# Kernel optimization log

Hardware: AMD Instinct MI355X
Metric: run time of the kernel (lower is better)

Reference implementation:

```python
import jax, jax.numpy as jnp
import numpy as np

N_NODES = 50000
N_EDGES = 800000
D = 128
N_LAYERS = 5  # 1 input + 3 hidden + 1 output MaxAggConv layers


def setup_inputs() -> dict:
    key = jax.random.key(0)
    k1, k2, k3, k4 = jax.random.split(key, 4)
    x = jax.random.normal(k1, (N_NODES, D), dtype=jnp.float32)
    edge_index = jax.random.randint(k2, (2, N_EDGES), 0, N_NODES, dtype=jnp.int64)
    # Linear params per layer (all layers are D->D here): W [out,in], b [out]
    Ws = jax.random.normal(k3, (N_LAYERS, D, D), dtype=jnp.float32) * (1.0 / np.sqrt(D))
    bs = jax.random.normal(k4, (N_LAYERS, D), dtype=jnp.float32) * 0.01
    return {"x": x, "edge_index": edge_index, "Ws": Ws, "bs": bs}


def _max_agg_conv(x, src, dst, W, b, n_nodes):
    # Linear: x @ W^T + b  (nn.Linear convention)
    h = jnp.einsum('nd,od->no', x, W) + b
    # gather per-edge messages x_j (source nodes), scatter-max into targets
    m = jax.ops.segment_max(h[src], dst, num_segments=n_nodes)
    # PyG scatter-max fills nodes with no incoming edges with 0
    return jnp.where(jnp.isneginf(m), 0.0, m)


def reference(x, edge_index, Ws, bs):
    src = edge_index[0]
    dst = edge_index[1]
    n = x.shape[0]
    for i in range(N_LAYERS - 1):
        x = _max_agg_conv(x, src, dst, Ws[i], bs[i], n)
        x = jax.nn.silu(x)
    x = _max_agg_conv(x, src, dst, Ws[N_LAYERS - 1], bs[N_LAYERS - 1], n)
    return x
```

## Files before the change

kernel.cpp:

```cpp
#include <hip/hip_runtime.h>
#include <hip/hip_bf16.h>
#include <hip/hip_fp16.h>
#include <math.h>

#define DF 128
#define NLAYERS 5

typedef __attribute__((ext_vector_type(8))) short bf16x8;
typedef __attribute__((ext_vector_type(4))) short short4v;
typedef __attribute__((ext_vector_type(4))) float f32x4;

__device__ inline unsigned short f2bf(float f) {
    unsigned u = __float_as_uint(f);
    u += 0x7FFF + ((u >> 16) & 1u);
    return (unsigned short)(u >> 16);
}
__device__ inline float bf2f(unsigned short s) {
    return __uint_as_float(((unsigned)s) << 16);
}

__device__ inline unsigned pkmax(unsigned a, unsigned b) {
    unsigned d;
    asm("v_pk_max_f16 %0, %1, %2" : "=v"(d) : "v"(a), "v"(b));
    return d;
}
__device__ inline float h2f(unsigned short u) {
    __half_raw r; r.x = u;
    return __half2float(__half(r));
}


__global__ void hist_rank_kernel(const int* __restrict__ dst, int* __restrict__ cnt,
        int* __restrict__ rank, int E) {
    int i = blockIdx.x * blockDim.x + threadIdx.x;
    if (i < E) rank[i] = atomicAdd(&cnt[dst[i]], 1);
}

__global__ __launch_bounds__(256) void partial_sum_kernel(const int* __restrict__ cnt,
        int* __restrict__ bsum, int n) {
    __shared__ int red[256];
    int t = threadIdx.x;
    int i = blockIdx.x * 256 + t;
    red[t] = (i < n) ? cnt[i] : 0;
    __syncthreads();
    for (int d = 128; d > 0; d >>= 1) {
        if (t < d) red[t] += red[t + d];
        __syncthreads();
    }
    if (t == 0) bsum[blockIdx.x] = red[0];
}

__global__ __launch_bounds__(1024) void scan_bsums_kernel(const int* __restrict__ bsum,
        int* __restrict__ bbase, int nb) {
    __shared__ int s[1024];
    int t = threadIdx.x;
    int v = (t < nb) ? bsum[t] : 0;
    s[t] = v;
    __syncthreads();
    for (int d = 1; d < 1024; d <<= 1) {
        int u = (t >= d) ? s[t - d] : 0;
        __syncthreads();
        s[t] += u;
        __syncthreads();
    }
    if (t < nb) bbase[t] = s[t] - v;
}

__global__ __launch_bounds__(256) void scan_scatter_kernel(const int* __restrict__ cnt,
        const int* __restrict__ bbase, int* __restrict__ off, int n, int E) {
    __shared__ int s[256];
    int t = threadIdx.x;
    int i = blockIdx.x * 256 + t;
    int v = (i < n) ? cnt[i] : 0;
    s[t] = v;
    __syncthreads();
    for (int d = 1; d < 256; d <<= 1) {
        int u = (t >= d) ? s[t - d] : 0;
        __syncthreads();
        s[t] += u;
        __syncthreads();
    }
    int excl = s[t] - v + bbase[blockIdx.x];
    if (i < n) off[i] = excl;
    if (blockIdx.x == 0 && t == 0) off[n] = E;
}

__global__ void fill_kernel(const int* __restrict__ src, const int* __restrict__ dst,
        const int* __restrict__ off, const int* __restrict__ rank,
        int* __restrict__ csr, int E) {
    int i = blockIdx.x * blockDim.x + threadIdx.x;
    if (i < E) csr[off[dst[i]] + rank[i]] = src[i];
}


__global__ __launch_bounds__(256) void split_kernel(const float* __restrict__ in,
        short* __restrict__ hi, short* __restrict__ lo, int total4) {
    int i = blockIdx.x * 256 + threadIdx.x;
    if (i >= total4) return;
    float4 v = reinterpret_cast<const float4*>(in)[i];
    short4v h, l;
    {
        unsigned short a = f2bf(v.x); h.x = (short)a; l.x = (short)f2bf(v.x - bf2f(a));
        unsigned short b = f2bf(v.y); h.y = (short)b; l.y = (short)f2bf(v.y - bf2f(b));
        unsigned short c = f2bf(v.z); h.z = (short)c; l.z = (short)f2bf(v.z - bf2f(c));
        unsigned short d = f2bf(v.w); h.w = (short)d; l.w = (short)f2bf(v.w - bf2f(d));
    }
    reinterpret_cast<short4v*>(hi)[i] = h;
    reinterpret_cast<short4v*>(lo)[i] = l;
}


__global__ __launch_bounds__(256, 3) void gemm_mfma_kernel(
        const short* __restrict__ xhi, const short* __restrict__ xlo,
        const short* __restrict__ whi, const short* __restrict__ wlo,
        const float* __restrict__ bias, __half* __restrict__ h, int n) {
    int wave = threadIdx.x >> 6;
    int lane = threadIdx.x & 63;
    int wm = wave >> 1;
    int wn = wave & 1;
    int m0 = blockIdx.x * 64 + wm * 32;
    int n0 = wn * 64;
    int lr = lane & 15;
    int lk = lane >> 4;

    f32x4 acc[2][4];
#pragma unroll
    for (int mt = 0; mt < 2; ++mt)
#pragma unroll
        for (int nt = 0; nt < 4; ++nt) {
            float bv = bias[n0 + nt * 16 + lr];
            acc[mt][nt] = (f32x4){bv, bv, bv, bv};
        }

    int rowA0 = min(m0 + lr, n - 1);
    int rowA1 = min(m0 + 16 + lr, n - 1);

#pragma unroll
    for (int ks = 0; ks < 4; ++ks) {
        int ko = ks * 32 + lk * 8;
        bf16x8 a0h = *(const bf16x8*)(xhi + (size_t)rowA0 * DF + ko);
        bf16x8 a0l = *(const bf16x8*)(xlo + (size_t)rowA0 * DF + ko);
        bf16x8 a1h = *(const bf16x8*)(xhi + (size_t)rowA1 * DF + ko);
        bf16x8 a1l = *(const bf16x8*)(xlo + (size_t)rowA1 * DF + ko);
#pragma unroll
        for (int nt = 0; nt < 4; ++nt) {
            int ncol = n0 + nt * 16 + lr;
            bf16x8 bh = *(const bf16x8*)(whi + ncol * DF + ko);
            bf16x8 bl = *(const bf16x8*)(wlo + ncol * DF + ko);
            acc[0][nt] = __builtin_amdgcn_mfma_f32_16x16x32_bf16(a0h, bh, acc[0][nt], 0, 0, 0);
            acc[0][nt] = __builtin_amdgcn_mfma_f32_16x16x32_bf16(a0l, bh, acc[0][nt], 0, 0, 0);
            acc[0][nt] = __builtin_amdgcn_mfma_f32_16x16x32_bf16(a0h, bl, acc[0][nt], 0, 0, 0);
            acc[1][nt] = __builtin_amdgcn_mfma_f32_16x16x32_bf16(a1h, bh, acc[1][nt], 0, 0, 0);
            acc[1][nt] = __builtin_amdgcn_mfma_f32_16x16x32_bf16(a1l, bh, acc[1][nt], 0, 0, 0);
            acc[1][nt] = __builtin_amdgcn_mfma_f32_16x16x32_bf16(a1h, bl, acc[1][nt], 0, 0, 0);
        }
    }

#pragma unroll
    for (int mt = 0; mt < 2; ++mt) {
        int rbase = m0 + mt * 16 + lk * 4;
#pragma unroll
        for (int j = 0; j < 4; ++j) {
            int r = rbase + j;
            if (r < n) {
#pragma unroll
                for (int nt = 0; nt < 4; ++nt)
                    h[(size_t)r * DF + n0 + nt * 16 + lr] = __float2half(acc[mt][nt][j]);
            }
        }
    }
}


__global__ __launch_bounds__(256) void agg_kernel(const __half* __restrict__ h,
        const int* __restrict__ off, const int* __restrict__ csr,
        float* __restrict__ out, short* __restrict__ ohi, short* __restrict__ olo,
        int n, int split) {
    int wid = threadIdx.x >> 6;
    int lane = threadIdx.x & 63;
    int node = blockIdx.x * 4 + wid;
    if (node >= n) return;

    int hf = lane >> 5;
    int l = lane & 31;
    const uint2* h2 = (const uint2*)h;

    int beg = off[node];
    int end = off[node + 1];

    unsigned m0 = 0xFC00FC00u;
    unsigned m1 = 0xFC00FC00u;

    int k = beg;
    for (; k + 7 < end; k += 8) {
        int s0 = csr[k + 0 + hf];
        int s1 = csr[k + 2 + hf];
        int s2 = csr[k + 4 + hf];
        int s3 = csr[k + 6 + hf];
        uint2 a = h2[s0 * 32 + l];
        uint2 b = h2[s1 * 32 + l];
        uint2 c = h2[s2 * 32 + l];
        uint2 d = h2[s3 * 32 + l];
        m0 = pkmax(m0, pkmax(pkmax(a.x, b.x), pkmax(c.x, d.x)));
        m1 = pkmax(m1, pkmax(pkmax(a.y, b.y), pkmax(c.y, d.y)));
    }
    for (; k + 1 < end; k += 2) {
        int s0 = csr[k + hf];
        uint2 a = h2[s0 * 32 + l];
        m0 = pkmax(m0, a.x);
        m1 = pkmax(m1, a.y);
    }
    if (k < end && hf == 0) {
        uint2 a = h2[csr[k] * 32 + l];
        m0 = pkmax(m0, a.x);
        m1 = pkmax(m1, a.y);
    }

    m0 = pkmax(m0, (unsigned)__shfl_xor((int)m0, 32));
    m1 = pkmax(m1, (unsigned)__shfl_xor((int)m1, 32));

    if (hf != 0) return;

    float f0 = h2f((unsigned short)(m0 & 0xFFFF));
    float f1 = h2f((unsigned short)(m0 >> 16));
    float f2 = h2f((unsigned short)(m1 & 0xFFFF));
    float f3 = h2f((unsigned short)(m1 >> 16));
    if (beg == end) { f0 = f1 = f2 = f3 = 0.0f; }

    if (split) {
        f0 = f0 * (1.0f / (1.0f + __expf(-f0)));
        f1 = f1 * (1.0f / (1.0f + __expf(-f1)));
        f2 = f2 * (1.0f / (1.0f + __expf(-f2)));
        f3 = f3 * (1.0f / (1.0f + __expf(-f3)));
        short4v hv, lv;
        unsigned short a = f2bf(f0); hv.x = (short)a; lv.x = (short)f2bf(f0 - bf2f(a));
        unsigned short b = f2bf(f1); hv.y = (short)b; lv.y = (short)f2bf(f1 - bf2f(b));
        unsigned short c = f2bf(f2); hv.z = (short)c; lv.z = (short)f2bf(f2 - bf2f(c));
        unsigned short d = f2bf(f3); hv.w = (short)d; lv.w = (short)f2bf(f3 - bf2f(d));
        *reinterpret_cast<short4v*>(ohi + (size_t)node * DF + l * 4) = hv;
        *reinterpret_cast<short4v*>(olo + (size_t)node * DF + l * 4) = lv;
    } else {
        float4 v = make_float4(f0, f1, f2, f3);
        reinterpret_cast<float4*>(out)[node * 32 + l] = v;
    }
}


extern "C" void kernel_launch(void* const* d_in, const int* in_sizes, int n_in,
                              void* d_out, int out_size, void* d_ws, size_t ws_size,
                              hipStream_t stream) {
    const float* x  = (const float*)d_in[0];
    const int*   ei = (const int*)d_in[1];
    const float* Ws = (const float*)d_in[2];
    const float* bs = (const float*)d_in[3];
    float* out = (float*)d_out;

    int N = in_sizes[0] / DF;
    int E = in_sizes[1] / 2;
    const int* src = ei;
    const int* dst = ei + E;

    char* w = (char*)d_ws;
    auto carve = [&](size_t bytes) {
        char* p = w;
        w += (bytes + 255) & ~(size_t)255;
        return p;
    };
    int nb = (N + 255) / 256;
    int*    cnt   = (int*)carve((size_t)(N + 1) * sizeof(int));
    int*    off   = (int*)carve((size_t)(N + 1) * sizeof(int));
    int*    bsum  = (int*)carve((size_t)nb * sizeof(int));
    int*    bbase = (int*)carve((size_t)nb * sizeof(int));
    int*    rank  = (int*)carve((size_t)E * sizeof(int));
    int*    csr   = (int*)carve((size_t)E * sizeof(int));
    __half* h     = (__half*)carve((size_t)N * DF * sizeof(__half));
    short*  xhi   = (short*)carve((size_t)N * DF * sizeof(short));
    short*  xlo   = (short*)carve((size_t)N * DF * sizeof(short));
    short*  whi   = (short*)carve((size_t)NLAYERS * DF * DF * sizeof(short));
    short*  wlo   = (short*)carve((size_t)NLAYERS * DF * DF * sizeof(short));

    hipMemsetAsync(cnt, 0, (size_t)N * sizeof(int), stream);
    hist_rank_kernel<<<(E + 255) / 256, 256, 0, stream>>>(dst, cnt, rank, E);
    partial_sum_kernel<<<nb, 256, 0, stream>>>(cnt, bsum, N);
    scan_bsums_kernel<<<1, 1024, 0, stream>>>(bsum, bbase, nb);
    scan_scatter_kernel<<<nb, 256, 0, stream>>>(cnt, bbase, off, N, E);
    fill_kernel<<<(E + 255) / 256, 256, 0, stream>>>(src, dst, off, rank, csr, E);

    int xt4 = N * DF / 4;
    split_kernel<<<(xt4 + 255) / 256, 256, 0, stream>>>(x, xhi, xlo, xt4);
    int wt4 = NLAYERS * DF * DF / 4;
    split_kernel<<<(wt4 + 255) / 256, 256, 0, stream>>>(Ws, whi, wlo, wt4);

    int ggrid = (N + 63) / 64;
    int agrid = (N + 3) / 4;
    for (int layer = 0; layer < NLAYERS; ++layer) {
        const short* whl = whi + (size_t)layer * DF * DF;
        const short* wll = wlo + (size_t)layer * DF * DF;
        const float* bl = bs + (size_t)layer * DF;
        gemm_mfma_kernel<<<ggrid, 256, 0, stream>>>(xhi, xlo, whl, wll, bl, h, N);
        int split = (layer < NLAYERS - 1) ? 1 : 0;
        agg_kernel<<<agrid, 256, 0, stream>>>(h, off, csr, out, xhi, xlo, N, split);
    }
}
```

Before: 373.2 us.

## Fuse max-aggregation with next layer's GEMM via shared-memory tile

Each block gathers and max-reduces 64 nodes' neighbor features, applies SiLU and splits the result into bf16 hi/lo in swizzled LDS, then runs the next layer's MFMA GEMM directly from LDS. This removes the global write and re-read of the split activations between aggregation and GEMM, plus four kernel launches, using ping-pong fp16 buffers. The gather is also reworked to 16-byte loads with 16 lanes per row covering 8 edges per iteration. The cost is fewer waves doing gathers (16 nodes serial per wave) and a block-wide barrier before the GEMM, which may reduce latency hiding in the irregular gather.

New measurement: 392.3 us. +5.1%, slower.

```diff
diff --git a/kernel.cpp b/kernel.cpp
--- a/kernel.cpp
+++ b/kernel.cpp
@@ -27,6 +27,9 @@
 __device__ inline float h2f(unsigned short u) {
     __half_raw r; r.x = u;
     return __half2float(__half(r));
+}
+__device__ inline float silu(float v) {
+    return v * (1.0f / (1.0f + __expf(-v)));
 }
 
 
@@ -172,76 +175,173 @@
 }
 
 
-__global__ __launch_bounds__(256) void agg_kernel(const __half* __restrict__ h,
+__global__ __launch_bounds__(256) void fused_agg_gemm_kernel(
+        const __half* __restrict__ hin,
         const int* __restrict__ off, const int* __restrict__ csr,
-        float* __restrict__ out, short* __restrict__ ohi, short* __restrict__ olo,
-        int n, int split) {
-    int wid = threadIdx.x >> 6;
+        const short* __restrict__ whi, const short* __restrict__ wlo,
+        const float* __restrict__ bias, __half* __restrict__ hout, int n) {
+    __shared__ __align__(16) short xh[64 * DF];
+    __shared__ __align__(16) short xl[64 * DF];
+
+    int wave = threadIdx.x >> 6;
     int lane = threadIdx.x & 63;
-    int node = blockIdx.x * 4 + wid;
-    if (node >= n) return;
-
-    int hf = lane >> 5;
-    int l = lane & 31;
-    const uint2* h2 = (const uint2*)h;
-
-    int beg = off[node];
-    int end = off[node + 1];
-
-    unsigned m0 = 0xFC00FC00u;
-    unsigned m1 = 0xFC00FC00u;
-
-    int k = beg;
-    for (; k + 7 < end; k += 8) {
-        int s0 = csr[k + 0 + hf];
-        int s1 = csr[k + 2 + hf];
-        int s2 = csr[k + 4 + hf];
-        int s3 = csr[k + 6 + hf];
-        uint2 a = h2[s0 * 32 + l];
-        uint2 b = h2[s1 * 32 + l];
-        uint2 c = h2[s2 * 32 + l];
-        uint2 d = h2[s3 * 32 + l];
-        m0 = pkmax(m0, pkmax(pkmax(a.x, b.x), pkmax(c.x, d.x)));
-        m1 = pkmax(m1, pkmax(pkmax(a.y, b.y), pkmax(c.y, d.y)));
-    }
-    for (; k + 1 < end; k += 2) {
-        int s0 = csr[k + hf];
-        uint2 a = h2[s0 * 32 + l];
-        m0 = pkmax(m0, a.x);
-        m1 = pkmax(m1, a.y);
-    }
-    if (k < end && hf == 0) {
-        uint2 a = h2[csr[k] * 32 + l];
-        m0 = pkmax(m0, a.x);
-        m1 = pkmax(m1, a.y);
-    }
-
-    m0 = pkmax(m0, (unsigned)__shfl_xor((int)m0, 32));
-    m1 = pkmax(m1, (unsigned)__shfl_xor((int)m1, 32));
-
-    if (hf != 0) return;
-
-    float f0 = h2f((unsigned short)(m0 & 0xFFFF));
-    float f1 = h2f((unsigned short)(m0 >> 16));
-    float f2 = h2f((unsigned short)(m1 & 0xFFFF));
-    float f3 = h2f((unsigned short)(m1 >> 16));
-    if (beg == end) { f0 = f1 = f2 = f3 = 0.0f; }
-
-    if (split) {
-        f0 = f0 * (1.0f / (1.0f + __expf(-f0)));
-        f1 = f1 * (1.0f / (1.0f + __expf(-f1)));
-        f2 = f2 * (1.0f / (1.0f + __expf(-f2)));
-        f3 = f3 * (1.0f / (1.0f + __expf(-f3)));
-        short4v hv, lv;
-        unsigned short a = f2bf(f0); hv.x = (short)a; lv.x = (short)f2bf(f0 - bf2f(a));
-        unsigned short b = f2bf(f1); hv.y = (short)b; lv.y = (short)f2bf(f1 - bf2f(b));
-        unsigned short c = f2bf(f2); hv.z = (short)c; lv.z = (short)f2bf(f2 - bf2f(c));
-        unsigned short d = f2bf(f3); hv.w = (short)d; lv.w = (short)f2bf(f3 - bf2f(d));
-        *reinterpret_cast<short4v*>(ohi + (size_t)node * DF + l * 4) = hv;
-        *reinterpret_cast<short4v*>(olo + (size_t)node * DF + l * 4) = lv;
-    } else {
-        float4 v = make_float4(f0, f1, f2, f3);
-        reinterpret_cast<float4*>(out)[node * 32 + l] = v;
+    int q = lane >> 4;
+    int c = lane & 15;
+    int nodebase = blockIdx.x * 64;
+
+    for (int i = 0; i < 16; ++i) {
+        int r = wave * 16 + i;
+        int node = nodebase + r;
+        if (node >= n) break;
+        int beg = off[node];
+        int end = off[node + 1];
+        unsigned m0 = 0xFC00FC00u, m1 = m0, m2 = m0, m3 = m0;
+        if (beg < end) {
+            for (int k = beg; k < end; k += 8) {
+                int ka = min(k + q, end - 1);
+                int kb = min(k + 4 + q, end - 1);
+                uint4 a = *(const uint4*)((const char*)hin + ((size_t)csr[ka] << 8) + (c << 4));
+                uint4 b = *(const uint4*)((const char*)hin + ((size_t)csr[kb] << 8) + (c << 4));
+                m0 = pkmax(m0, pkmax(a.x, b.x));
+                m1 = pkmax(m1, pkmax(a.y, b.y));
+                m2 = pkmax(m2, pkmax(a.z, b.z));
+                m3 = pkmax(m3, pkmax(a.w, b.w));
+            }
+            m0 = pkmax(m0, (unsigned)__shfl_xor((int)m0, 16));
+            m0 = pkmax(m0, (unsigned)__shfl_xor((int)m0, 32));
+            m1 = pkmax(m1, (unsigned)__shfl_xor((int)m1, 16));
+            m1 = pkmax(m1, (unsigned)__shfl_xor((int)m1, 32));
+            m2 = pkmax(m2, (unsigned)__shfl_xor((int)m2, 16));
+            m2 = pkmax(m2, (unsigned)__shfl_xor((int)m2, 32));
+            m3 = pkmax(m3, (unsigned)__shfl_xor((int)m3, 16));
+            m3 = pkmax(m3, (unsigned)__shfl_xor((int)m3, 32));
+        }
+        if (q == 0) {
+            float f[8];
+            f[0] = h2f((unsigned short)(m0 & 0xFFFF)); f[1] = h2f((unsigned short)(m0 >> 16));
+            f[2] = h2f((unsigned short)(m1 & 0xFFFF)); f[3] = h2f((unsigned short)(m1 >> 16));
+            f[4] = h2f((unsigned short)(m2 & 0xFFFF)); f[5] = h2f((unsigned short)(m2 >> 16));
+            f[6] = h2f((unsigned short)(m3 & 0xFFFF)); f[7] = h2f((unsigned short)(m3 >> 16));
+            bf16x8 hv, lv;
+#pragma unroll
+            for (int j = 0; j < 8; ++j) {
+                float v = (beg == end) ? 0.0f : silu(f[j]);
+                unsigned short a = f2bf(v);
+                hv[j] = (short)a;
+                lv[j] = (short)f2bf(v - bf2f(a));
+            }
+            int bc = (c << 4) ^ ((r & 7) << 4);
+            *(bf16x8*)((char*)xh + r * 256 + bc) = hv;
+            *(bf16x8*)((char*)xl + r * 256 + bc) = lv;
+        }
+    }
+    __syncthreads();
+
+    int wm = wave >> 1;
+    int wn = wave & 1;
+    int n0 = wn * 64;
+    int lr = lane & 15;
+    int lk = lane >> 4;
+
+    f32x4 acc[2][4];
+#pragma unroll
+    for (int mt = 0; mt < 2; ++mt)
+#pragma unroll
+        for (int nt = 0; nt < 4; ++nt) {
+            float bv = bias[n0 + nt * 16 + lr];
+            acc[mt][nt] = (f32x4){bv, bv, bv, bv};
+        }
+
+    int row0 = wm * 32 + lr;
+    int row1 = row0 + 16;
+
+#pragma unroll
+    for (int ks = 0; ks < 4; ++ks) {
+        int bo = ks * 64 + lk * 16;
+        bf16x8 a0h = *(const bf16x8*)((char*)xh + row0 * 256 + (bo ^ ((row0 & 7) << 4)));
+        bf16x8 a0l = *(const bf16x8*)((char*)xl + row0 * 256 + (bo ^ ((row0 & 7) << 4)));
+        bf16x8 a1h = *(const bf16x8*)((char*)xh + row1 * 256 + (bo ^ ((row1 & 7) << 4)));
+        bf16x8 a1l = *(const bf16x8*)((char*)xl + row1 * 256 + (bo ^ ((row1 & 7) << 4)));
+        int ko = ks * 32 + lk * 8;
+#pragma unroll
+        for (int nt = 0; nt < 4; ++nt) {
+            int ncol = n0 + nt * 16 + lr;
+            bf16x8 bh = *(const bf16x8*)(whi + ncol * DF + ko);
+            bf16x8 bl = *(const bf16x8*)(wlo + ncol * DF + ko);
+            acc[0][nt] = __builtin_amdgcn_mfma_f32_16x16x32_bf16(a0h, bh, acc[0][nt], 0, 0, 0);
+            acc[0][nt] = __builtin_amdgcn_mfma_f32_16x16x32_bf16(a0l, bh, acc[0][nt], 0, 0, 0);
+            acc[0][nt] = __builtin_amdgcn_mfma_f32_16x16x32_bf16(a0h, bl, acc[0][nt], 0, 0, 0);
+            acc[1][nt] = __builtin_amdgcn_mfma_f32_16x16x32_bf16(a1h, bh, acc[1][nt], 0, 0, 0);
+            acc[1][nt] = __builtin_amdgcn_mfma_f32_16x16x32_bf16(a1l, bh, acc[1][nt], 0, 0, 0);
+            acc[1][nt] = __builtin_amdgcn_mfma_f32_16x16x32_bf16(a1h, bl, acc[1][nt], 0, 0, 0);
+        }
+    }
+
+#pragma unroll
+    for (int mt = 0; mt < 2; ++mt) {
+        int rbase = nodebase + wm * 32 + mt * 16 + lk * 4;
+#pragma unroll
+        for (int j = 0; j < 4; ++j) {
+            int r = rbase + j;
+            if (r < n) {
+#pragma unroll
+                for (int nt = 0; nt < 4; ++nt)
+                    hout[(size_t)r * DF + n0 + nt * 16 + lr] = __float2half(acc[mt][nt][j]);
+            }
+        }
+    }
+}
+
+
+__global__ __launch_bounds__(256) void agg_final_kernel(const __half* __restrict__ hin,
+        const int* __restrict__ off, const int* __restrict__ csr,
+        float* __restrict__ out, int n) {
+    int wave = threadIdx.x >> 6;
+    int lane = threadIdx.x & 63;
+    int q = lane >> 4;
+    int c = lane & 15;
+    int nodebase = blockIdx.x * 64;
+
+    for (int i = 0; i < 16; ++i) {
+        int node = nodebase + wave * 16 + i;
+        if (node >= n) break;
+        int beg = off[node];
+        int end = off[node + 1];
+        unsigned m0 = 0xFC00FC00u, m1 = m0, m2 = m0, m3 = m0;
+        if (beg < end) {
+            for (int k = beg; k < end; k += 8) {
+                int ka = min(k + q, end - 1);
+                int kb = min(k + 4 + q, end - 1);
+                uint4 a = *(const uint4*)((const char*)hin + ((size_t)csr[ka] << 8) + (c << 4));
+                uint4 b = *(const uint4*)((const char*)hin + ((size_t)csr[kb] << 8) + (c << 4));
+                m0 = pkmax(m0, pkmax(a.x, b.x));
+                m1 = pkmax(m1, pkmax(a.y, b.y));
+                m2 = pkmax(m2, pkmax(a.z, b.z));
+                m3 = pkmax(m3, pkmax(a.w, b.w));
+            }
+            m0 = pkmax(m0, (unsigned)__shfl_xor((int)m0, 16));
+            m0 = pkmax(m0, (unsigned)__shfl_xor((int)m0, 32));
+            m1 = pkmax(m1, (unsigned)__shfl_xor((int)m1, 16));
+            m1 = pkmax(m1, (unsigned)__shfl_xor((int)m1, 32));
+            m2 = pkmax(m2, (unsigned)__shfl_xor((int)m2, 16));
+            m2 = pkmax(m2, (unsigned)__shfl_xor((int)m2, 32));
+            m3 = pkmax(m3, (unsigned)__shfl_xor((int)m3, 16));
+            m3 = pkmax(m3, (unsigned)__shfl_xor((int)m3, 32));
+        }
+        if (q == 0) {
+            float f[8];
+            f[0] = h2f((unsigned short)(m0 & 0xFFFF)); f[1] = h2f((unsigned short)(m0 >> 16));
+            f[2] = h2f((unsigned short)(m1 & 0xFFFF)); f[3] = h2f((unsigned short)(m1 >> 16));
+            f[4] = h2f((unsigned short)(m2 & 0xFFFF)); f[5] = h2f((unsigned short)(m2 >> 16));
+            f[6] = h2f((unsigned short)(m3 & 0xFFFF)); f[7] = h2f((unsigned short)(m3 >> 16));
+            if (beg == end) {
+#pragma unroll
+                for (int j = 0; j < 8; ++j) f[j] = 0.0f;
+            }
+            float4* o = (float4*)(out + (size_t)node * DF + c * 8);
+            o[0] = make_float4(f[0], f[1], f[2], f[3]);
+            o[1] = make_float4(f[4], f[5], f[6], f[7]);
+        }
     }
 }
 
@@ -273,7 +373,8 @@
     int*    bbase = (int*)carve((size_t)nb * sizeof(int));
     int*    rank  = (int*)carve((size_t)E * sizeof(int));
     int*    csr   = (int*)carve((size_t)E * sizeof(int));
-    __half* h     = (__half*)carve((size_t)N * DF * sizeof(__half));
+    __half* hA    = (__half*)carve((size_t)N * DF * sizeof(__half));
+    __half* hB    = (__half*)carve((size_t)N * DF * sizeof(__half));
     short*  xhi   = (short*)carve((size_t)N * DF * sizeof(short));
     short*  xlo   = (short*)carve((size_t)N * DF * sizeof(short));
     short*  whi   = (short*)carve((size_t)NLAYERS * DF * DF * sizeof(short));
@@ -291,14 +392,20 @@
     int wt4 = NLAYERS * DF * DF / 4;
     split_kernel<<<(wt4 + 255) / 256, 256, 0, stream>>>(Ws, whi, wlo, wt4);
 
-    int ggrid = (N + 63) / 64;
-    int agrid = (N + 3) / 4;
-    for (int layer = 0; layer < NLAYERS; ++layer) {
+    int nblocks = (N + 63) / 64;
+
+    gemm_mfma_kernel<<<nblocks, 256, 0, stream>>>(xhi, xlo, whi, wlo, bs, hA, N);
+
+    __half* hin = hA;
+    __half* hout = hB;
+    for (int layer = 1; layer < NLAYERS; ++layer) {
         const short* whl = whi + (size_t)layer * DF * DF;
         const short* wll = wlo + (size_t)layer * DF * DF;
         const float* bl = bs + (size_t)layer * DF;
-        gemm_mfma_kernel<<<ggrid, 256, 0, stream>>>(xhi, xlo, whl, wll, bl, h, N);
-        int split = (layer < NLAYERS - 1) ? 1 : 0;
-        agg_kernel<<<agrid, 256, 0, stream>>>(h, off, csr, out, xhi, xlo, N, split);
-    }
-}
+        fused_agg_gemm_kernel<<<nblocks, 256, 0, stream>>>(
+            hin, off, csr, whl, wll, bl, hout, N);
+        __half* t = hin; hin = hout; hout = t;
+    }
+
+    agg_final_kernel<<<nblocks, 256, 0, stream>>>(hin, off, csr, out, N);
+}
```

## Fuse input split into first GEMM, merge prep kernels, widen aggregation unroll

Applied to the files above, without the earlier changes.

The separate fp32-to-bf16 hi/lo split of x is removed: a new first-layer GEMM reads fp32 x directly and splits it in registers. The histogram/rank pass and the weight split are merged into one launch to save a kernel launch. The aggregation loop now processes 16 edges per iteration with clamped indices instead of 8-edge, 2-edge and tail loops, which raises memory-level parallelism but issues redundant loads for low-degree nodes.

New measurement: 346.7 us. -7.1%, faster.

```diff
diff --git a/kernel.cpp b/kernel.cpp
--- a/kernel.cpp
+++ b/kernel.cpp
@@ -28,13 +28,47 @@
     __half_raw r; r.x = u;
     return __half2float(__half(r));
 }
-
-
-__global__ void hist_rank_kernel(const int* __restrict__ dst, int* __restrict__ cnt,
-        int* __restrict__ rank, int E) {
-    int i = blockIdx.x * blockDim.x + threadIdx.x;
-    if (i < E) rank[i] = atomicAdd(&cnt[dst[i]], 1);
-}
+__device__ inline float silu(float v) {
+    return v * (1.0f / (1.0f + __expf(-v)));
+}
+
+__device__ inline void split8(const float* p, bf16x8& hi, bf16x8& lo) {
+    float4 v0 = *reinterpret_cast<const float4*>(p);
+    float4 v1 = *reinterpret_cast<const float4*>(p + 4);
+    float f[8] = {v0.x, v0.y, v0.z, v0.w, v1.x, v1.y, v1.z, v1.w};
+#pragma unroll
+    for (int j = 0; j < 8; ++j) {
+        unsigned short a = f2bf(f[j]);
+        hi[j] = (short)a;
+        lo[j] = (short)f2bf(f[j] - bf2f(a));
+    }
+}
+
+
+__global__ __launch_bounds__(256) void prep_kernel(const int* __restrict__ dst,
+        int* __restrict__ cnt, int* __restrict__ rank, int E, int nbE,
+        const float* __restrict__ Ws, short* __restrict__ whi,
+        short* __restrict__ wlo, int wt4) {
+    int b = blockIdx.x;
+    int t = threadIdx.x;
+    if (b < nbE) {
+        int i = b * 256 + t;
+        if (i < E) rank[i] = atomicAdd(&cnt[dst[i]], 1);
+    } else {
+        int i = (b - nbE) * 256 + t;
+        if (i < wt4) {
+            float4 v = reinterpret_cast<const float4*>(Ws)[i];
+            short4v h, l;
+            unsigned short a = f2bf(v.x); h.x = (short)a; l.x = (short)f2bf(v.x - bf2f(a));
+            unsigned short bq = f2bf(v.y); h.y = (short)bq; l.y = (short)f2bf(v.y - bf2f(bq));
+            unsigned short c = f2bf(v.z); h.z = (short)c; l.z = (short)f2bf(v.z - bf2f(c));
+            unsigned short d = f2bf(v.w); h.w = (short)d; l.w = (short)f2bf(v.w - bf2f(d));
+            reinterpret_cast<short4v*>(whi)[i] = h;
+            reinterpret_cast<short4v*>(wlo)[i] = l;
+        }
+    }
+}
+
 
 __global__ __launch_bounds__(256) void partial_sum_kernel(const int* __restrict__ cnt,
         int* __restrict__ bsum, int n) {
@@ -93,20 +127,64 @@
 }
 
 
-__global__ __launch_bounds__(256) void split_kernel(const float* __restrict__ in,
-        short* __restrict__ hi, short* __restrict__ lo, int total4) {
-    int i = blockIdx.x * 256 + threadIdx.x;
-    if (i >= total4) return;
-    float4 v = reinterpret_cast<const float4*>(in)[i];
-    short4v h, l;
-    {
-        unsigned short a = f2bf(v.x); h.x = (short)a; l.x = (short)f2bf(v.x - bf2f(a));
-        unsigned short b = f2bf(v.y); h.y = (short)b; l.y = (short)f2bf(v.y - bf2f(b));
-        unsigned short c = f2bf(v.z); h.z = (short)c; l.z = (short)f2bf(v.z - bf2f(c));
-        unsigned short d = f2bf(v.w); h.w = (short)d; l.w = (short)f2bf(v.w - bf2f(d));
-    }
-    reinterpret_cast<short4v*>(hi)[i] = h;
-    reinterpret_cast<short4v*>(lo)[i] = l;
+__global__ __launch_bounds__(256, 3) void gemm0_kernel(
+        const float* __restrict__ x,
+        const short* __restrict__ whi, const short* __restrict__ wlo,
+        const float* __restrict__ bias, __half* __restrict__ h, int n) {
+    int wave = threadIdx.x >> 6;
+    int lane = threadIdx.x & 63;
+    int wm = wave >> 1;
+    int wn = wave & 1;
+    int m0 = blockIdx.x * 64 + wm * 32;
+    int n0 = wn * 64;
+    int lr = lane & 15;
+    int lk = lane >> 4;
+
+    f32x4 acc[2][4];
+#pragma unroll
+    for (int mt = 0; mt < 2; ++mt)
+#pragma unroll
+        for (int nt = 0; nt < 4; ++nt) {
+            float bv = bias[n0 + nt * 16 + lr];
+            acc[mt][nt] = (f32x4){bv, bv, bv, bv};
+        }
+
+    int rowA0 = min(m0 + lr, n - 1);
+    int rowA1 = min(m0 + 16 + lr, n - 1);
+
+#pragma unroll
+    for (int ks = 0; ks < 4; ++ks) {
+        int ko = ks * 32 + lk * 8;
+        bf16x8 a0h, a0l, a1h, a1l;
+        split8(x + (size_t)rowA0 * DF + ko, a0h, a0l);
+        split8(x + (size_t)rowA1 * DF + ko, a1h, a1l);
+#pragma unroll
+        for (int nt = 0; nt < 4; ++nt) {
+            int ncol = n0 + nt * 16 + lr;
+            bf16x8 bh = *(const bf16x8*)(whi + ncol * DF + ko);
+            bf16x8 bl = *(const bf16x8*)(wlo + ncol * DF + ko);
+            acc[0][nt] = __builtin_amdgcn_mfma_f32_16x16x32_bf16(a0h, bh, acc[0][nt], 0, 0, 0);
+            acc[0][nt] = __builtin_amdgcn_mfma_f32_16x16x32_bf16(a0l, bh, acc[0][nt], 0, 0, 0);
+            acc[0][nt] = __builtin_amdgcn_mfma_f32_16x16x32_bf16(a0h, bl, acc[0][nt], 0, 0, 0);
+            acc[1][nt] = __builtin_amdgcn_mfma_f32_16x16x32_bf16(a1h, bh, acc[1][nt], 0, 0, 0);
+            acc[1][nt] = __builtin_amdgcn_mfma_f32_16x16x32_bf16(a1l, bh, acc[1][nt], 0, 0, 0);
+            acc[1][nt] = __builtin_amdgcn_mfma_f32_16x16x32_bf16(a1h, bl, acc[1][nt], 0, 0, 0);
+        }
+    }
+
+#pragma unroll
+    for (int mt = 0; mt < 2; ++mt) {
+        int rbase = m0 + mt * 16 + lk * 4;
+#pragma unroll
+        for (int j = 0; j < 4; ++j) {
+            int r = rbase + j;
+            if (r < n) {
+#pragma unroll
+                for (int nt = 0; nt < 4; ++nt)
+                    h[(size_t)r * DF + n0 + nt * 16 + lr] = __float2half(acc[mt][nt][j]);
+            }
+        }
+    }
 }
 
 
@@ -172,7 +250,7 @@
 }
 
 
-__global__ __launch_bounds__(256) void agg_kernel(const __half* __restrict__ h,
+__global__ __launch_bounds__(256) void agg_kernel(const __half* __restrict__ hin,
         const int* __restrict__ off, const int* __restrict__ csr,
         float* __restrict__ out, short* __restrict__ ohi, short* __restrict__ olo,
         int n, int split) {
@@ -183,7 +261,7 @@
 
     int hf = lane >> 5;
     int l = lane & 31;
-    const uint2* h2 = (const uint2*)h;
+    const uint2* h2 = (const uint2*)hin;
 
     int beg = off[node];
     int end = off[node + 1];
@@ -191,29 +269,27 @@
     unsigned m0 = 0xFC00FC00u;
     unsigned m1 = 0xFC00FC00u;
 
-    int k = beg;
-    for (; k + 7 < end; k += 8) {
-        int s0 = csr[k + 0 + hf];
-        int s1 = csr[k + 2 + hf];
-        int s2 = csr[k + 4 + hf];
-        int s3 = csr[k + 6 + hf];
-        uint2 a = h2[s0 * 32 + l];
-        uint2 b = h2[s1 * 32 + l];
-        uint2 c = h2[s2 * 32 + l];
-        uint2 d = h2[s3 * 32 + l];
-        m0 = pkmax(m0, pkmax(pkmax(a.x, b.x), pkmax(c.x, d.x)));
-        m1 = pkmax(m1, pkmax(pkmax(a.y, b.y), pkmax(c.y, d.y)));
-    }
-    for (; k + 1 < end; k += 2) {
-        int s0 = csr[k + hf];
-        uint2 a = h2[s0 * 32 + l];
-        m0 = pkmax(m0, a.x);
-        m1 = pkmax(m1, a.y);
-    }
-    if (k < end && hf == 0) {
-        uint2 a = h2[csr[k] * 32 + l];
-        m0 = pkmax(m0, a.x);
-        m1 = pkmax(m1, a.y);
+    int e1 = end - 1;
+    for (int k = beg; k < end; k += 16) {
+        int k0 = k + hf;
+        int i0 = min(k0,      e1), i1 = min(k0 + 2,  e1);
+        int i2 = min(k0 + 4,  e1), i3 = min(k0 + 6,  e1);
+        int i4 = min(k0 + 8,  e1), i5 = min(k0 + 10, e1);
+        int i6 = min(k0 + 12, e1), i7 = min(k0 + 14, e1);
+        int s0 = csr[i0], s1 = csr[i1], s2 = csr[i2], s3 = csr[i3];
+        int s4 = csr[i4], s5 = csr[i5], s6 = csr[i6], s7 = csr[i7];
+        uint2 a0 = h2[s0 * 32 + l];
+        uint2 a1 = h2[s1 * 32 + l];
+        uint2 a2 = h2[s2 * 32 + l];
+        uint2 a3 = h2[s3 * 32 + l];
+        uint2 a4 = h2[s4 * 32 + l];
+        uint2 a5 = h2[s5 * 32 + l];
+        uint2 a6 = h2[s6 * 32 + l];
+        uint2 a7 = h2[s7 * 32 + l];
+        m0 = pkmax(m0, pkmax(pkmax(pkmax(a0.x, a1.x), pkmax(a2.x, a3.x)),
+                             pkmax(pkmax(a4.x, a5.x), pkmax(a6.x, a7.x))));
+        m1 = pkmax(m1, pkmax(pkmax(pkmax(a0.y, a1.y), pkmax(a2.y, a3.y)),
+                             pkmax(pkmax(a4.y, a5.y), pkmax(a6.y, a7.y))));
     }
 
     m0 = pkmax(m0, (unsigned)__shfl_xor((int)m0, 32));
@@ -228,10 +304,7 @@
     if (beg == end) { f0 = f1 = f2 = f3 = 0.0f; }
 
     if (split) {
-        f0 = f0 * (1.0f / (1.0f + __expf(-f0)));
-        f1 = f1 * (1.0f / (1.0f + __expf(-f1)));
-        f2 = f2 * (1.0f / (1.0f + __expf(-f2)));
-        f3 = f3 * (1.0f / (1.0f + __expf(-f3)));
+        f0 = silu(f0); f1 = silu(f1); f2 = silu(f2); f3 = silu(f3);
         short4v hv, lv;
         unsigned short a = f2bf(f0); hv.x = (short)a; lv.x = (short)f2bf(f0 - bf2f(a));
         unsigned short b = f2bf(f1); hv.y = (short)b; lv.y = (short)f2bf(f1 - bf2f(b));
@@ -280,25 +353,26 @@
     short*  wlo   = (short*)carve((size_t)NLAYERS * DF * DF * sizeof(short));
 
     hipMemsetAsync(cnt, 0, (size_t)N * sizeof(int), stream);
-    hist_rank_kernel<<<(E + 255) / 256, 256, 0, stream>>>(dst, cnt, rank, E);
+    int nbE = (E + 255) / 256;
+    int wt4 = NLAYERS * DF * DF / 4;
+    int nbW = (wt4 + 255) / 256;
+    prep_kernel<<<nbE + nbW, 256, 0, stream>>>(dst, cnt, rank, E, nbE, Ws, whi, wlo, wt4);
     partial_sum_kernel<<<nb, 256, 0, stream>>>(cnt, bsum, N);
     scan_bsums_kernel<<<1, 1024, 0, stream>>>(bsum, bbase, nb);
     scan_scatter_kernel<<<nb, 256, 0, stream>>>(cnt, bbase, off, N, E);
-    fill_kernel<<<(E + 255) / 256, 256, 0, stream>>>(src, dst, off, rank, csr, E);
-
-    int xt4 = N * DF / 4;
-    split_kernel<<<(xt4 + 255) / 256, 256, 0, stream>>>(x, xhi, xlo, xt4);
-    int wt4 = NLAYERS * DF * DF / 4;
-    split_kernel<<<(wt4 + 255) / 256, 256, 0, stream>>>(Ws, whi, wlo, wt4);
+    fill_kernel<<<nbE, 256, 0, stream>>>(src, dst, off, rank, csr, E);
 
     int ggrid = (N + 63) / 64;
     int agrid = (N + 3) / 4;
-    for (int layer = 0; layer < NLAYERS; ++layer) {
+
+    gemm0_kernel<<<ggrid, 256, 0, stream>>>(x, whi, wlo, bs, h, N);
+
+    for (int layer = 1; layer < NLAYERS; ++layer) {
+        agg_kernel<<<agrid, 256, 0, stream>>>(h, off, csr, out, xhi, xlo, N, 1);
         const short* whl = whi + (size_t)layer * DF * DF;
         const short* wll = wlo + (size_t)layer * DF * DF;
         const float* bl = bs + (size_t)layer * DF;
         gemm_mfma_kernel<<<ggrid, 256, 0, stream>>>(xhi, xlo, whl, wll, bl, h, N);
-        int split = (layer < NLAYERS - 1) ? 1 : 0;
-        agg_kernel<<<agrid, 256, 0, stream>>>(h, off, csr, out, xhi, xlo, N, split);
-    }
-}
+    }
+    agg_kernel<<<agrid, 256, 0, stream>>>(h, off, csr, out, NULL, NULL, N, 0);
+}
```
